# Optimization experiments

Hardware: AMD Instinct MI355X
Metric: run time of the kernel (lower is better)

## Reference

```python
import jax, jax.numpy as jnp
import numpy as np

B, E, F = 16384, 128, 6
ITEM_V, CATE_V, HIST = 91718, 11, 50
I_IDX, J_IDX = np.triu_indices(F, k=1)  # 15 field pairs, loop order (0,1),(0,2),...
EPS = 1e-5


def _xavier(key, shape):
    fan_in, fan_out = shape[0], shape[-1]
    std = (2.0 / (fan_in + fan_out)) ** 0.5
    return std * jax.random.normal(key, shape, dtype=jnp.float32)


def setup_inputs() -> dict:
    key = jax.random.key(0)
    ks = jax.random.split(key, 20)
    inp = {
        'item_id': jax.random.randint(ks[0], (B,), 0, ITEM_V),
        'item_emb_d128': jax.random.normal(ks[1], (B, 128), dtype=jnp.float32),
        'likes_level': jax.random.randint(ks[2], (B,), 0, CATE_V),
        'views_level': jax.random.randint(ks[3], (B,), 0, CATE_V),
        'item_seq': jax.random.randint(ks[4], (B, HIST), 0, ITEM_V),
        # learned parameters
        'item_emb': 0.05 * jax.random.normal(ks[5], (ITEM_V, E), dtype=jnp.float32),
        'cate_emb': 0.05 * jax.random.normal(ks[6], (CATE_V, E), dtype=jnp.float32),
        'mm_W': _xavier(ks[7], (128, E)), 'mm_b': jnp.zeros((E,), jnp.float32),
        'ln_g': jnp.ones((E,), jnp.float32), 'ln_b': jnp.zeros((E,), jnp.float32),
        'se_W1': _xavier(ks[8], (F, F // 2)), 'se_b1': jnp.zeros((F // 2,), jnp.float32),
        'se_W2': _xavier(ks[9], (F // 2, F)), 'se_b2': jnp.zeros((F,), jnp.float32),
        'bi_W': _xavier(ks[10], (E, E)),
        'mlp_W1': _xavier(ks[11], (21 * E, 512)), 'mlp_b1': jnp.zeros((512,), jnp.float32),
        'bn1_g': jnp.ones((512,), jnp.float32), 'bn1_b': jnp.zeros((512,), jnp.float32),
        'bn1_rm': jnp.zeros((512,), jnp.float32), 'bn1_rv': jnp.ones((512,), jnp.float32),
        'mlp_W2': _xavier(ks[12], (512, 256)), 'mlp_b2': jnp.zeros((256,), jnp.float32),
        'bn2_g': jnp.ones((256,), jnp.float32), 'bn2_b': jnp.zeros((256,), jnp.float32),
        'bn2_rm': jnp.zeros((256,), jnp.float32), 'bn2_rv': jnp.ones((256,), jnp.float32),
        'mlp_W3': _xavier(ks[13], (256, 1)), 'mlp_b3': jnp.zeros((1,), jnp.float32),
    }
    return inp


def _forward(item_id, item_emb_d128, likes_level, views_level, item_seq,
             item_emb, cate_emb, mm_W, mm_b, ln_g, ln_b,
             se_W1, se_b1, se_W2, se_b2, bi_W,
             mlp_W1, mlp_b1, bn1_g, bn1_b, bn1_rm, bn1_rv,
             mlp_W2, mlp_b2, bn2_g, bn2_b, bn2_rm, bn2_rv,
             mlp_W3, mlp_b3):
    b = item_id.shape[0]
    tab = item_emb.at[0].set(0.0)  # padding_idx=0
    like_feat = cate_emb[likes_level]
    view_feat = cate_emb[views_level]
    item_feat = tab[item_id]
    # mm_proj: Linear -> LayerNorm -> ReLU
    mm = item_emb_d128 @ mm_W + mm_b
    mu = mm.mean(-1, keepdims=True)
    var = jnp.var(mm, axis=-1, keepdims=True)
    mm = jax.nn.relu((mm - mu) / jnp.sqrt(var + EPS) * ln_g + ln_b)
    # masked mean pooling over history
    seq_emb = tab[item_seq]                               # (B, HIST, E)
    valid = (item_seq != 0).astype(seq_emb.dtype)
    seq_sum = (seq_emb * valid[..., None]).sum(1)
    cnt = jnp.clip(valid.sum(1, keepdims=True), 1.0)
    hist_feat = seq_sum / cnt
    user_feat = jnp.zeros((b, E), seq_emb.dtype)
    x = jnp.stack([user_feat, like_feat, view_feat, item_feat, mm, hist_feat], axis=1)  # (B,6,E)
    # SENet
    z = x.mean(-1)
    w = jax.nn.sigmoid(jax.nn.relu(z @ se_W1 + se_b1) @ se_W2 + se_b2)
    xs = x * w[:, :, None]
    # bilinear 'all'
    xw = jnp.einsum('bfe,ed->bfd', xs, bi_W)
    p = xs[:, I_IDX, :] * xw[:, J_IDX, :]                 # (B,15,E)
    c = jnp.concatenate([xs.reshape(b, -1), p.reshape(b, -1)], axis=1)  # (B, 2688)
    # MLP head (eval mode: BN uses running stats, dropout off)
    h = c @ mlp_W1 + mlp_b1
    h = jax.nn.relu((h - bn1_rm) / jnp.sqrt(bn1_rv + EPS) * bn1_g + bn1_b)
    h = h @ mlp_W2 + mlp_b2
    h = jax.nn.relu((h - bn2_rm) / jnp.sqrt(bn2_rv + EPS) * bn2_g + bn2_b)
    logits = h @ mlp_W3 + mlp_b3
    return jax.nn.sigmoid(logits)[:, 0]


def reference(item_id, item_emb_d128, likes_level, views_level, item_seq,
              item_emb, cate_emb, mm_W, mm_b, ln_g, ln_b,
              se_W1, se_b1, se_W2, se_b2, bi_W,
              mlp_W1, mlp_b1, bn1_g, bn1_b, bn1_rm, bn1_rv,
              mlp_W2, mlp_b2, bn2_g, bn2_b, bn2_rm, bn2_rv,
              mlp_W3, mlp_b3):
    return _forward(item_id, item_emb_d128, likes_level, views_level, item_seq,
                    item_emb, cate_emb, mm_W, mm_b, ln_g, ln_b,
                    se_W1, se_b1, se_W2, se_b2, bi_W,
                    mlp_W1, mlp_b1, bn1_g, bn1_b, bn1_rm, bn1_rv,
                    mlp_W2, mlp_b2, bn2_g, bn2_b, bn2_rm, bn2_rv,
                    mlp_W3, mlp_b3)
```

## Files before the change

### kernel.cpp

```cpp
#include <hip/hip_runtime.h>
#include <hip/hip_bf16.h>

typedef __hip_bfloat16 bfloat;
typedef __bf16 bf16x8 __attribute__((ext_vector_type(8)));
typedef float f32x4 __attribute__((ext_vector_type(4)));

#define B_SZ   16384
#define E_DIM  128
#define HIST_L 50


__device__ __constant__ int ISL[10] = {0,0,0,0,1,1,1,2,2,3};

__device__ __forceinline__ void gl_lds16(const void* g, void* l) {
    __builtin_amdgcn_global_load_lds(
        (const __attribute__((address_space(1))) unsigned int*)g,
        (__attribute__((address_space(3))) unsigned int*)l, 16, 0, 0);
}

template<int TB>
__global__ __launch_bounds__(256) void feat_kernel(
    const int* __restrict__ item_id,
    const int* __restrict__ likes, const int* __restrict__ views,
    const int* __restrict__ seq,
    const void* __restrict__ item_tab, const float* __restrict__ cate_emb,
    const float* __restrict__ mm,
    const float* __restrict__ ln_g, const float* __restrict__ ln_b,
    const float* __restrict__ se_W1, const float* __restrict__ se_b1,
    const float* __restrict__ se_W2, const float* __restrict__ se_b2,
    bfloat* __restrict__ xs)
{
    const int tid = threadIdx.x;
    const int r   = tid >> 7;
    const int e   = tid & 127;
    const int b   = blockIdx.x * 2 + r;
    const int w   = tid >> 6;

    __shared__ float redh[2][4][128];
    __shared__ int   seq_s[2][64];
    __shared__ float lnred[4], lnred2[4];
    __shared__ float zred[5][4];
    __shared__ float wsh[2][6];
    __shared__ int   cnt_s[2];

    if (e < 64) seq_s[r][e] = (e < HIST_L) ? seq[(size_t)b * HIST_L + e] : 0;
    __syncthreads();

    const int iid = item_id[b];
    const float like_v = cate_emb[likes[b] * 128 + e];
    const float view_v = cate_emb[views[b] * 128 + e];
    float item_v;
    if (TB) {
        const bfloat* tb = (const bfloat*)item_tab;
        item_v = __bfloat162float(tb[(size_t)iid * 128 + e]);
    } else {
        const float* tf = (const float*)item_tab;
        float raw = tf[(size_t)iid * 128 + e];
        item_v = iid ? raw : 0.f;
    }
    const float acc = mm[(size_t)b * 128 + e];

    const int q   = e >> 5;
    const int l32 = e & 31;
    float4 hs = make_float4(0.f, 0.f, 0.f, 0.f);
    if (TB) {
        const ushort* tb = (const ushort*)item_tab;
        #pragma unroll
        for (int g = 0; g < 13; ++g) {
            int s = seq_s[r][g * 4 + q];
            ushort4 v = *(const ushort4*)&tb[(size_t)s * 128 + l32 * 4];
            hs.x += __bfloat162float(__ushort_as_bfloat16(v.x));
            hs.y += __bfloat162float(__ushort_as_bfloat16(v.y));
            hs.z += __bfloat162float(__ushort_as_bfloat16(v.z));
            hs.w += __bfloat162float(__ushort_as_bfloat16(v.w));
        }
    } else {
        const float* tf = (const float*)item_tab;
        #pragma unroll
        for (int g = 0; g < 13; ++g) {
            int s = seq_s[r][g * 4 + q];
            const float4 v = *(const float4*)&tf[(size_t)s * 128 + l32 * 4];
            float m = (s != 0) ? 1.f : 0.f;
            hs.x = fmaf(v.x, m, hs.x);
            hs.y = fmaf(v.y, m, hs.y);
            hs.z = fmaf(v.z, m, hs.z);
            hs.w = fmaf(v.w, m, hs.w);
        }
    }

    {
        float v = acc;
        #pragma unroll
        for (int off = 32; off > 0; off >>= 1) v += __shfl_down(v, off, 64);
        if ((tid & 63) == 0) lnred[w] = v;
    }
    __syncthreads();
    const float mu = (lnred[2 * r] + lnred[2 * r + 1]) * (1.f / 128.f);
    const float d  = acc - mu;
    {
        float v = d * d;
        #pragma unroll
        for (int off = 32; off > 0; off >>= 1) v += __shfl_down(v, off, 64);
        if ((tid & 63) == 0) lnred2[w] = v;
    }
    redh[r][q][l32 * 4 + 0] = hs.x;
    redh[r][q][l32 * 4 + 1] = hs.y;
    redh[r][q][l32 * 4 + 2] = hs.z;
    redh[r][q][l32 * 4 + 3] = hs.w;
    if ((w & 1) == 0 && e < 64) {
        bool valid = (e < HIST_L) && (seq_s[r][e] != 0);
        unsigned long long m = __ballot(valid);
        if (e == 0) cnt_s[r] = (int)__popcll(m);
    }
    __syncthreads();
    const float var = (lnred2[2 * r] + lnred2[2 * r + 1]) * (1.f / 128.f);
    float xmm = d * rsqrtf(var + 1e-5f) * ln_g[e] + ln_b[e];
    xmm = fmaxf(xmm, 0.f);

    const int cnt = cnt_s[r] > 0 ? cnt_s[r] : 1;
    const float hist_v = (redh[r][0][e] + redh[r][1][e] +
                          redh[r][2][e] + redh[r][3][e]) / (float)cnt;

    {
        float s1 = like_v, s2 = view_v, s3 = item_v, s4 = xmm, s5 = hist_v;
        #pragma unroll
        for (int off = 32; off > 0; off >>= 1) {
            s1 += __shfl_down(s1, off, 64);
            s2 += __shfl_down(s2, off, 64);
            s3 += __shfl_down(s3, off, 64);
            s4 += __shfl_down(s4, off, 64);
            s5 += __shfl_down(s5, off, 64);
        }
        if ((tid & 63) == 0) {
            zred[0][w] = s1; zred[1][w] = s2; zred[2][w] = s3;
            zred[3][w] = s4; zred[4][w] = s5;
        }
    }
    __syncthreads();

    if (e == 0) {
        float z[6];
        z[0] = 0.f;
        #pragma unroll
        for (int f = 1; f < 6; ++f)
            z[f] = (zred[f - 1][2 * r] + zred[f - 1][2 * r + 1]) * (1.f / 128.f);
        float a[3];
        #pragma unroll
        for (int j = 0; j < 3; ++j) {
            float s = se_b1[j];
            #pragma unroll
            for (int f = 0; f < 6; ++f) s += z[f] * se_W1[f * 3 + j];
            a[j] = fmaxf(s, 0.f);
        }
        #pragma unroll
        for (int f = 0; f < 6; ++f) {
            float s = se_b2[f];
            #pragma unroll
            for (int j = 0; j < 3; ++j) s += a[j] * se_W2[j * 6 + f];
            wsh[r][f] = 1.f / (1.f + expf(-s));
        }
    }
    __syncthreads();

    bfloat* xrow = xs + (size_t)b * 640;
    xrow[0 * 128 + e] = __float2bfloat16(like_v * wsh[r][1]);
    xrow[1 * 128 + e] = __float2bfloat16(view_v * wsh[r][2]);
    xrow[2 * 128 + e] = __float2bfloat16(item_v * wsh[r][3]);
    xrow[3 * 128 + e] = __float2bfloat16(xmm    * wsh[r][4]);
    xrow[4 * 128 + e] = __float2bfloat16(hist_v * wsh[r][5]);
}

__global__ __launch_bounds__(256) void transpose_W1c(
    const float* __restrict__ W1, bfloat* __restrict__ W1t)
{
    __shared__ float t[64][65];
    const int tid = threadIdx.x;
    const int kk0 = blockIdx.x * 64, n0 = blockIdx.y * 64;
    const int j = tid & 63;
    #pragma unroll
    for (int p = 0; p < 16; ++p) {
        int i = (tid >> 6) + p * 4;
        int kk = kk0 + i;
        int orig = kk + (kk < 640 ? 128 : 768);
        t[i][j] = W1[(size_t)orig * 512 + n0 + j];
    }
    __syncthreads();
    #pragma unroll
    for (int p = 0; p < 16; ++p) {
        int i = (tid >> 6) + p * 4;
        W1t[(size_t)(n0 + i) * 1920 + kk0 + j] = __float2bfloat16(t[j][i]);
    }
}

__global__ __launch_bounds__(256) void prep_kernel(
    const float* __restrict__ W2, const float* __restrict__ bi_W,
    const float* __restrict__ mm_W,
    bfloat* __restrict__ W2t, bfloat* __restrict__ bWt,
    bfloat* __restrict__ mmWt,
    const float* __restrict__ lb1, const float* __restrict__ g1,
    const float* __restrict__ bb1, const float* __restrict__ rm1,
    const float* __restrict__ rv1,
    const float* __restrict__ lb2, const float* __restrict__ g2,
    const float* __restrict__ bb2, const float* __restrict__ rm2,
    const float* __restrict__ rv2,
    const float* __restrict__ mm_b,
    float* __restrict__ S1, float* __restrict__ T1,
    float* __restrict__ S2, float* __restrict__ T2,
    float* __restrict__ Tmm)
{
    int idx = blockIdx.x * 256 + threadIdx.x;
    if (idx < 131072) {
        int k = idx >> 8, n = idx & 255;
        W2t[(size_t)n * 512 + k] = __float2bfloat16(W2[idx]);
    } else if (idx < 147456) {
        int t = idx - 131072;
        int k = t >> 7, n = t & 127;
        bWt[n * 128 + k] = __float2bfloat16(bi_W[t]);
    } else if (idx < 163840) {
        int t = idx - 147456;
        int k = t >> 7, n = t & 127;
        mmWt[n * 128 + k] = __float2bfloat16(mm_W[t]);
    } else if (idx < 164352) {
        int j = idx - 163840;
        float s = g1[j] * rsqrtf(rv1[j] + 1e-5f);
        S1[j] = s;
        T1[j] = (lb1[j] - rm1[j]) * s + bb1[j];
    } else if (idx < 164608) {
        int j = idx - 164352;
        float s = g2[j] * rsqrtf(rv2[j] + 1e-5f);
        S2[j] = s;
        T2[j] = (lb2[j] - rm2[j]) * s + bb2[j];
    } else if (idx < 164736) {
        int j = idx - 164608;
        Tmm[j] = mm_b[j];
    }
}

__global__ __launch_bounds__(256) void cvt_emb(
    const float* __restrict__ in, bfloat* __restrict__ out, int n8)
{
    int idx = blockIdx.x * 256 + threadIdx.x;
    if (idx >= n8) return;
    if (idx < 16) {
        union { bf16x8 v; unsigned short s[8]; } z;
        #pragma unroll
        for (int i = 0; i < 8; ++i) z.s[i] = 0;
        ((bf16x8*)out)[idx] = z.v;
        return;
    }
    float4 f0 = ((const float4*)in)[idx * 2];
    float4 f1 = ((const float4*)in)[idx * 2 + 1];
    union { bf16x8 v; unsigned short s[8]; } u;
    u.s[0] = __bfloat16_as_ushort(__float2bfloat16(f0.x));
    u.s[1] = __bfloat16_as_ushort(__float2bfloat16(f0.y));
    u.s[2] = __bfloat16_as_ushort(__float2bfloat16(f0.z));
    u.s[3] = __bfloat16_as_ushort(__float2bfloat16(f0.w));
    u.s[4] = __bfloat16_as_ushort(__float2bfloat16(f1.x));
    u.s[5] = __bfloat16_as_ushort(__float2bfloat16(f1.y));
    u.s[6] = __bfloat16_as_ushort(__float2bfloat16(f1.z));
    u.s[7] = __bfloat16_as_ushort(__float2bfloat16(f1.w));
    ((bf16x8*)out)[idx] = u.v;
}

__global__ __launch_bounds__(256, 1) void gemm_mlp1(
    const bfloat* __restrict__ Axs, const bfloat* __restrict__ Ap,
    const bfloat* __restrict__ Bt, bfloat* __restrict__ C,
    int M, int N, int K,
    const float* __restrict__ S, const float* __restrict__ T)
{
    extern __shared__ __align__(16) short smem[];

    const int tid  = threadIdx.x;
    const int bm   = blockIdx.x * 256;
    const int bn   = blockIdx.y * 128;
    const int wave = tid >> 6;
    const int lane = tid & 63;
    const int wm   = (wave >> 1) * 128;
    const int wn   = (wave & 1) * 64;

    const short* Ag  = (const short*)Axs;
    const short* A2g = (const short*)Ap;
    const short* Bg  = (const short*)Bt;

    f32x4 acc[8][4];
    #pragma unroll
    for (int i = 0; i < 8; ++i)
        #pragma unroll
        for (int j = 0; j < 4; ++j)
            acc[i][j] = (f32x4){0.f, 0.f, 0.f, 0.f};

    const int l8  = lane >> 3;
    const int gch = (lane & 7) ^ l8;

    auto stage = [&](int buf, int kt) {
        short* Ab = smem + buf * 24576;
        short* Bb = Ab + 16384;
        #pragma unroll
        for (int d = 0; d < 4; ++d) {
            int seg = wave * 4 + d;
            int row = seg * 8 + l8;
            gl_lds16(&Bg[(long)(bn + row) * K + kt + gch * 8],
                     &Bb[seg * 512 + lane * 8]);
        }
        #pragma unroll
        for (int d = 0; d < 8; ++d) {
            int seg = wave * 8 + d;
            int row = seg * 8 + l8;
            long rb = (long)(bm + row);
            const short* src = (kt < 640)
                ? &Ag [rb * 640  + kt + gch * 8]
                : &A2g[rb * 1280 + (kt - 640) + gch * 8];
            gl_lds16(src, &Ab[seg * 512 + lane * 8]);
        }
    };

    const int rbase = lane & 15;
    const int rsw   = rbase & 7;

    const int nk = K >> 6;
    stage(0, 0);
    stage(1, 64);

    for (int i = 0; i < nk; ++i) {
        if (i + 1 < nk) asm volatile("s_waitcnt vmcnt(12)" ::: "memory");
        else            asm volatile("s_waitcnt vmcnt(0)" ::: "memory");
        __builtin_amdgcn_s_barrier();
        __builtin_amdgcn_sched_barrier(0);

        if (i + 2 < nk) stage((i + 2) % 3, (i + 2) << 6);

        const short* Ab = smem + (i % 3) * 24576;
        const short* Bb = Ab + 16384;
        #pragma unroll
        for (int h = 0; h < 2; ++h) {
            const int cg = h * 4 + (lane >> 4);
            const int ca = (cg ^ rsw) << 3;
            bf16x8 af[8], bfr[4];
            #pragma unroll
            for (int mt = 0; mt < 8; ++mt)
                af[mt] = *(const bf16x8*)
                    &Ab[(wm + mt * 16 + rbase) * 64 + ca];
            #pragma unroll
            for (int nt = 0; nt < 4; ++nt)
                bfr[nt] = *(const bf16x8*)
                    &Bb[(wn + nt * 16 + rbase) * 64 + ca];
            #pragma unroll
            for (int mt = 0; mt < 8; ++mt)
                #pragma unroll
                for (int nt = 0; nt < 4; ++nt)
                    acc[mt][nt] = __builtin_amdgcn_mfma_f32_16x16x32_bf16(
                        af[mt], bfr[nt], acc[mt][nt], 0, 0, 0);
        }
    }

    const int col0 = lane & 15;
    const int row0 = (lane >> 4) * 4;
    #pragma unroll
    for (int nt = 0; nt < 4; ++nt) {
        int col = bn + wn + nt * 16 + col0;
        float s = S[col], t = T[col];
        #pragma unroll
        for (int mt = 0; mt < 8; ++mt) {
            #pragma unroll
            for (int i = 0; i < 4; ++i) {
                int row = bm + wm + mt * 16 + row0 + i;
                float v = fmaxf(acc[mt][nt][i] * s + t, 0.f);
                C[(size_t)row * N + col] = __float2bfloat16(v);
            }
        }
    }
}

template<int MODE, int EPI, int F32OUT>
__global__ __launch_bounds__(256, 2) void gemm_bt(
    const void* __restrict__ A, const bfloat* __restrict__ A2,
    const bfloat* __restrict__ Bt, void* __restrict__ C,
    int M, int N, int K,
    const float* __restrict__ S, const float* __restrict__ T)
{
    __shared__ __align__(16) short As[4][128 * 32];
    __shared__ __align__(16) short Bs[4][128 * 32];

    const int tid  = threadIdx.x;
    const int bm   = blockIdx.x * 128;
    const int bn   = blockIdx.y * 128;
    const int wave = tid >> 6;
    const int lane = tid & 63;
    const int wm   = (wave >> 1) * 64;
    const int wn   = (wave & 1) * 64;

    const short* Ag  = (const short*)A;
    const short* A2g = (const short*)A2;
    const short* Bg  = (const short*)Bt;

    f32x4 acc[4][4];
    #pragma unroll
    for (int i = 0; i < 4; ++i)
        #pragma unroll
        for (int j = 0; j < 4; ++j)
            acc[i][j] = (f32x4){0.f, 0.f, 0.f, 0.f};

    const int srow = tid >> 2;
    const int sck  = tid & 3;

    auto stage = [&](int buf, int kt) {
        #pragma unroll
        for (int rr = 0; rr < 2; ++rr) {
            int row = srow + rr * 64;
            int g   = sck ^ ((row >> 1) & 3);
            gl_lds16(&Bg[(long)(bn + row) * K + kt + g * 8],
                     &Bs[buf][row * 32 + sck * 8]);
        }
        if (MODE == 3) {
            const float* Af = (const float*)A;
            #pragma unroll
            for (int rr = 0; rr < 2; ++rr) {
                int row = srow + rr * 64;
                int g   = sck ^ ((row >> 1) & 3);
                long aoff = (long)(bm + row) * K + kt + g * 8;
                float4 f0 = *(const float4*)&Af[aoff];
                float4 f1 = *(const float4*)&Af[aoff + 4];
                union { bf16x8 v; unsigned short s[8]; } u;
                u.s[0] = __bfloat16_as_ushort(__float2bfloat16(f0.x));
                u.s[1] = __bfloat16_as_ushort(__float2bfloat16(f0.y));
                u.s[2] = __bfloat16_as_ushort(__float2bfloat16(f0.z));
                u.s[3] = __bfloat16_as_ushort(__float2bfloat16(f0.w));
                u.s[4] = __bfloat16_as_ushort(__float2bfloat16(f1.x));
                u.s[5] = __bfloat16_as_ushort(__float2bfloat16(f1.y));
                u.s[6] = __bfloat16_as_ushort(__float2bfloat16(f1.z));
                u.s[7] = __bfloat16_as_ushort(__float2bfloat16(f1.w));
                *(bf16x8*)&As[buf][row * 32 + sck * 8] = u.v;
            }
        } else {
            #pragma unroll
            for (int rr = 0; rr < 2; ++rr) {
                int row = srow + rr * 64;
                int g   = sck ^ ((row >> 1) & 3);
                const short* src;
                if (MODE == 2) {
                    int gr = bm + row;
                    src = &Ag[((long)(gr >> 2)) * 640 +
                              ((gr & 3) + 1) * 128 + kt + g * 8];
                } else {
                    src = &Ag[(long)(bm + row) * K + kt + g * 8];
                }
                gl_lds16(src, &As[buf][row * 32 + sck * 8]);
            }
        }
    };

    const int rbase = lane & 15;
    const int cg    = lane >> 4;
    const int ca    = (cg ^ ((rbase >> 1) & 3)) << 3;

    const int nk = K >> 5;
    stage(0, 0);
    stage(1, 32);
    if (nk > 2) stage(2, 64);

    for (int i = 0; i < nk; ++i) {
        if (MODE == 3)
            asm volatile("s_waitcnt vmcnt(0) lgkmcnt(0)" ::: "memory");
        else if (i + 2 < nk)
            asm volatile("s_waitcnt vmcnt(8)" ::: "memory");
        else if (i + 1 < nk)
            asm volatile("s_waitcnt vmcnt(4)" ::: "memory");
        else
            asm volatile("s_waitcnt vmcnt(0)" ::: "memory");
        __builtin_amdgcn_s_barrier();
        __builtin_amdgcn_sched_barrier(0);

        const int cur = i & 3;
        bf16x8 af[4], bfr[4];
        #pragma unroll
        for (int mt = 0; mt < 4; ++mt)
            af[mt] = *(const bf16x8*)
                &As[cur][(wm + mt * 16 + rbase) * 32 + ca];
        #pragma unroll
        for (int nt = 0; nt < 4; ++nt)
            bfr[nt] = *(const bf16x8*)
                &Bs[cur][(wn + nt * 16 + rbase) * 32 + ca];
        #pragma unroll
        for (int mt = 0; mt < 4; ++mt)
            #pragma unroll
            for (int nt = 0; nt < 4; ++nt)
                acc[mt][nt] = __builtin_amdgcn_mfma_f32_16x16x32_bf16(
                    af[mt], bfr[nt], acc[mt][nt], 0, 0, 0);

        if (i + 3 < nk) stage((i + 3) & 3, (i + 3) << 5);
    }

    const int col0 = lane & 15;
    const int row0 = (lane >> 4) * 4;
    #pragma unroll
    for (int nt = 0; nt < 4; ++nt) {
        int col = bn + wn + nt * 16 + col0;
        float s = 1.f, t = 0.f;
        if (EPI == 1 || EPI == 2) { s = (EPI == 1) ? S[col] : 1.f; t = T[col]; }
        #pragma unroll
        for (int mt = 0; mt < 4; ++mt) {
            #pragma unroll
            for (int i = 0; i < 4; ++i) {
                int row = bm + wm + mt * 16 + row0 + i;
                float v = acc[mt][nt][i];
                if (EPI == 3) {
                    const bfloat* xsp = (const bfloat*)A;
                    bfloat* Pp = (bfloat*)C;
                    long b = row >> 2;
                    int pplist[4];
                    int npp;
                    if (i == 0)      { npp = 1; pplist[0] = 0; }
                    else if (i == 1) { npp = 2; pplist[0] = 1; pplist[1] = 4; }
                    else if (i == 2) { npp = 3; pplist[0] = 2; pplist[1] = 5; pplist[2] = 7; }
                    else             { npp = 4; pplist[0] = 3; pplist[1] = 6; pplist[2] = 8; pplist[3] = 9; }
                    #pragma unroll
                    for (int t2 = 0; t2 < npp; ++t2) {
                        int pp  = pplist[t2];
                        int isl = ISL[pp];
                        float xv = __bfloat162float(
                            xsp[b * 640 + isl * 128 + col]);
                        Pp[b * 1280 + pp * 128 + col] =
                            __float2bfloat16(xv * v);
                    }
                } else {
                    if (EPI == 1) v = fmaxf(v * s + t, 0.f);
                    if (EPI == 2) v = v + t;
                    if (F32OUT) ((float*)C)[(size_t)row * N + col] = v;
                    else ((bfloat*)C)[(size_t)row * N + col] = __float2bfloat16(v);
                }
            }
        }
    }
}

__global__ __launch_bounds__(256) void head_kernel(
    const bfloat* __restrict__ h2, const float* __restrict__ W3,
    const float* __restrict__ b3, float* __restrict__ out)
{
    int lane = threadIdx.x & 63;
    int row  = blockIdx.x * 4 + (threadIdx.x >> 6);
    float acc = 0.f;
    #pragma unroll
    for (int i = 0; i < 4; ++i)
        acc += __bfloat162float(h2[(size_t)row * 256 + i * 64 + lane]) *
               W3[i * 64 + lane];
    #pragma unroll
    for (int off = 32; off > 0; off >>= 1) acc += __shfl_down(acc, off, 64);
    if (lane == 0) {
        float l = acc + b3[0];
        out[row] = 1.f / (1.f + expf(-l));
    }
}

extern "C" void kernel_launch(void* const* d_in, const int* in_sizes, int n_in,
                              void* d_out, int out_size, void* d_ws, size_t ws_size,
                              hipStream_t stream) {
    const int*   item_id = (const int*)  d_in[0];
    const float* d128    = (const float*)d_in[1];
    const int*   likes   = (const int*)  d_in[2];
    const int*   views   = (const int*)  d_in[3];
    const int*   seq     = (const int*)  d_in[4];
    const float* item_emb= (const float*)d_in[5];
    const float* cate_emb= (const float*)d_in[6];
    const float* mm_W    = (const float*)d_in[7];
    const float* mm_b    = (const float*)d_in[8];
    const float* ln_g    = (const float*)d_in[9];
    const float* ln_b    = (const float*)d_in[10];
    const float* se_W1   = (const float*)d_in[11];
    const float* se_b1   = (const float*)d_in[12];
    const float* se_W2   = (const float*)d_in[13];
    const float* se_b2   = (const float*)d_in[14];
    const float* bi_W    = (const float*)d_in[15];
    const float* W1      = (const float*)d_in[16];
    const float* b1      = (const float*)d_in[17];
    const float* bn1_g   = (const float*)d_in[18];
    const float* bn1_b   = (const float*)d_in[19];
    const float* bn1_rm  = (const float*)d_in[20];
    const float* bn1_rv  = (const float*)d_in[21];
    const float* W2      = (const float*)d_in[22];
    const float* b2      = (const float*)d_in[23];
    const float* bn2_g   = (const float*)d_in[24];
    const float* bn2_b   = (const float*)d_in[25];
    const float* bn2_rm  = (const float*)d_in[26];
    const float* bn2_rv  = (const float*)d_in[27];
    const float* W3      = (const float*)d_in[28];
    const float* b3      = (const float*)d_in[29];

    const size_t fixed = 2300416;
    const size_t ITB   = 23479808;
    int CH; bool use_tb;
    if      (fixed + ITB + (size_t)16384 * 4864 <= ws_size) { CH = 16384; use_tb = true;  }
    else if (fixed + (size_t)16384 * 4864 <= ws_size)       { CH = 16384; use_tb = false; }
    else if (fixed + ITB + (size_t)8192 * 4864 <= ws_size)  { CH = 8192;  use_tb = true;  }
    else if (fixed + (size_t)8192 * 4864 <= ws_size)        { CH = 8192;  use_tb = false; }
    else if (fixed + ITB + (size_t)4096 * 4864 <= ws_size)  { CH = 4096;  use_tb = true;  }
    else if (fixed + (size_t)4096 * 4864 <= ws_size)        { CH = 4096;  use_tb = false; }
    else if (fixed + (size_t)2048 * 4864 <= ws_size)        { CH = 2048;  use_tb = false; }
    else                                                    { CH = 1024;  use_tb = false; }

    char* ws = (char*)d_ws;
    bfloat* W1t = (bfloat*)(ws);
    bfloat* W2t = (bfloat*)(ws + 1966080);
    bfloat* bWt = (bfloat*)(ws + 2228224);
    bfloat* mmWt= (bfloat*)(ws + 2260992);
    float*  S1  = (float*) (ws + 2293760);
    float*  T1  = (float*) (ws + 2295808);
    float*  S2  = (float*) (ws + 2297856);
    float*  T2  = (float*) (ws + 2298880);
    float*  Tmm = (float*) (ws + 2299904);
    bfloat* itemb = (bfloat*)(ws + fixed);
    char*   cb  = ws + fixed + (use_tb ? ITB : 0);
    bfloat* xs  = (bfloat*)(cb);
    bfloat* h1  = (bfloat*)(cb + (size_t)CH * 1280);
    bfloat* P   = (bfloat*)(cb + (size_t)CH * 2304);
    float*  mm  = (float*)P;
    bfloat* h2  = (bfloat*)P;

    transpose_W1c<<<dim3(30, 8), 256, 0, stream>>>(W1, W1t);
    prep_kernel<<<(164736 + 255) / 256, 256, 0, stream>>>(
        W2, bi_W, mm_W, W2t, bWt, mmWt,
        b1, bn1_g, bn1_b, bn1_rm, bn1_rv,
        b2, bn2_g, bn2_b, bn2_rm, bn2_rv,
        mm_b, S1, T1, S2, T2, Tmm);
    if (use_tb) {
        const int n8 = 91718 * 128 / 8;
        cvt_emb<<<(n8 + 255) / 256, 256, 0, stream>>>(item_emb, itemb, n8);
    }

    for (int off = 0; off < B_SZ; off += CH) {
        dim3 gmm(CH / 128, 1);
        gemm_bt<3, 2, 1><<<gmm, 256, 0, stream>>>(
            d128 + (size_t)off * 128, nullptr, mmWt, mm,
            CH, 128, 128, nullptr, Tmm);

        if (use_tb)
            feat_kernel<1><<<CH / 2, 256, 0, stream>>>(
                item_id + off, likes + off, views + off,
                seq + (size_t)off * HIST_L, itemb, cate_emb, mm,
                ln_g, ln_b, se_W1, se_b1, se_W2, se_b2, xs);
        else
            feat_kernel<0><<<CH / 2, 256, 0, stream>>>(
                item_id + off, likes + off, views + off,
                seq + (size_t)off * HIST_L, item_emb, cate_emb, mm,
                ln_g, ln_b, se_W1, se_b1, se_W2, se_b2, xs);

        dim3 gxw(CH * 4 / 128, 1);
        gemm_bt<2, 3, 0><<<gxw, 256, 0, stream>>>(
            xs, nullptr, bWt, P, CH * 4, 128, 128, nullptr, nullptr);

        dim3 g1(CH / 256, 4);
        gemm_mlp1<<<g1, 256, 147456, stream>>>(
            xs, P, W1t, h1, CH, 512, 1920, S1, T1);

        dim3 g2(CH / 128, 2);
        gemm_bt<0, 1, 0><<<g2, 256, 0, stream>>>(
            h1, nullptr, W2t, h2, CH, 256, 512, S2, T2);

        head_kernel<<<CH / 4, 256, 0, stream>>>(h2, W3, b3, (float*)d_out + off);
    }
}
```

Baseline: 278.1 us.

## Fuse mm projection into feat kernel and merge prep kernels into one launch

The separate MFMA GEMM that projects item_emb_d128 through mm_W is removed. Each feat_kernel thread now computes its output element as a scalar 128-long dot product against a bf16 transposed weight row, reading the input row from LDS. This drops a launch and the fp32 mm intermediate round-trip through memory. The three setup kernels (W1 transpose, weight/BN prep, embedding conversion) are merged into one launch to cut launch overhead. The cost is that the projection now runs on scalar FMA instead of matrix cores, with each thread reading a 256-byte weight row.

```diff
diff --git a/kernel.cpp b/kernel.cpp
--- a/kernel.cpp
+++ b/kernel.cpp
@@ -24,7 +24,8 @@
     const int* __restrict__ likes, const int* __restrict__ views,
     const int* __restrict__ seq,
     const void* __restrict__ item_tab, const float* __restrict__ cate_emb,
-    const float* __restrict__ mm,
+    const float* __restrict__ d128, const bfloat* __restrict__ mmWt,
+    const float* __restrict__ mm_b,
     const float* __restrict__ ln_g, const float* __restrict__ ln_b,
     const float* __restrict__ se_W1, const float* __restrict__ se_b1,
     const float* __restrict__ se_W2, const float* __restrict__ se_b2,
@@ -37,6 +38,7 @@
     const int w   = tid >> 6;
 
     __shared__ float redh[2][4][128];
+    __shared__ float d128s[2][128];
     __shared__ int   seq_s[2][64];
     __shared__ float lnred[4], lnred2[4];
     __shared__ float zred[5][4];
@@ -44,6 +46,7 @@
     __shared__ int   cnt_s[2];
 
     if (e < 64) seq_s[r][e] = (e < HIST_L) ? seq[(size_t)b * HIST_L + e] : 0;
+    d128s[r][e] = d128[(size_t)b * 128 + e];
     __syncthreads();
 
     const int iid = item_id[b];
@@ -58,7 +61,6 @@
         float raw = tf[(size_t)iid * 128 + e];
         item_v = iid ? raw : 0.f;
     }
-    const float acc = mm[(size_t)b * 128 + e];
 
     const int q   = e >> 5;
     const int l32 = e & 31;
@@ -88,6 +90,22 @@
         }
     }
 
+    float acc = mm_b[e];
+    {
+        const ushort* wrow = (const ushort*)(mmWt + (size_t)e * 128);
+        #pragma unroll
+        for (int k8 = 0; k8 < 16; ++k8) {
+            union { bf16x8 v; ushort s[8]; } u;
+            u.v = *(const bf16x8*)&wrow[k8 * 8];
+            const float* dp = &d128s[r][k8 * 8];
+            #pragma unroll
+            for (int j = 0; j < 8; ++j)
+                acc = fmaf(dp[j],
+                           __bfloat162float(__ushort_as_bfloat16(u.s[j])),
+                           acc);
+        }
+    }
+
     {
         float v = acc;
         #pragma unroll
@@ -170,29 +188,8 @@
     xrow[4 * 128 + e] = __float2bfloat16(hist_v * wsh[r][5]);
 }
 
-__global__ __launch_bounds__(256) void transpose_W1c(
-    const float* __restrict__ W1, bfloat* __restrict__ W1t)
-{
-    __shared__ float t[64][65];
-    const int tid = threadIdx.x;
-    const int kk0 = blockIdx.x * 64, n0 = blockIdx.y * 64;
-    const int j = tid & 63;
-    #pragma unroll
-    for (int p = 0; p < 16; ++p) {
-        int i = (tid >> 6) + p * 4;
-        int kk = kk0 + i;
-        int orig = kk + (kk < 640 ? 128 : 768);
-        t[i][j] = W1[(size_t)orig * 512 + n0 + j];
-    }
-    __syncthreads();
-    #pragma unroll
-    for (int p = 0; p < 16; ++p) {
-        int i = (tid >> 6) + p * 4;
-        W1t[(size_t)(n0 + i) * 1920 + kk0 + j] = __float2bfloat16(t[j][i]);
-    }
-}
-
-__global__ __launch_bounds__(256) void prep_kernel(
+__global__ __launch_bounds__(256) void mega_prep(
+    const float* __restrict__ W1, bfloat* __restrict__ W1t,
     const float* __restrict__ W2, const float* __restrict__ bi_W,
     const float* __restrict__ mm_W,
     bfloat* __restrict__ W2t, bfloat* __restrict__ bWt,
@@ -203,63 +200,78 @@
     const float* __restrict__ lb2, const float* __restrict__ g2,
     const float* __restrict__ bb2, const float* __restrict__ rm2,
     const float* __restrict__ rv2,
-    const float* __restrict__ mm_b,
     float* __restrict__ S1, float* __restrict__ T1,
     float* __restrict__ S2, float* __restrict__ T2,
-    float* __restrict__ Tmm)
+    const float* __restrict__ item_emb, bfloat* __restrict__ itemb)
 {
-    int idx = blockIdx.x * 256 + threadIdx.x;
-    if (idx < 131072) {
-        int k = idx >> 8, n = idx & 255;
-        W2t[(size_t)n * 512 + k] = __float2bfloat16(W2[idx]);
-    } else if (idx < 147456) {
-        int t = idx - 131072;
-        int k = t >> 7, n = t & 127;
-        bWt[n * 128 + k] = __float2bfloat16(bi_W[t]);
-    } else if (idx < 163840) {
-        int t = idx - 147456;
-        int k = t >> 7, n = t & 127;
-        mmWt[n * 128 + k] = __float2bfloat16(mm_W[t]);
-    } else if (idx < 164352) {
-        int j = idx - 163840;
-        float s = g1[j] * rsqrtf(rv1[j] + 1e-5f);
-        S1[j] = s;
-        T1[j] = (lb1[j] - rm1[j]) * s + bb1[j];
-    } else if (idx < 164608) {
-        int j = idx - 164352;
-        float s = g2[j] * rsqrtf(rv2[j] + 1e-5f);
-        S2[j] = s;
-        T2[j] = (lb2[j] - rm2[j]) * s + bb2[j];
-    } else if (idx < 164736) {
-        int j = idx - 164608;
-        Tmm[j] = mm_b[j];
-    }
-}
-
-__global__ __launch_bounds__(256) void cvt_emb(
-    const float* __restrict__ in, bfloat* __restrict__ out, int n8)
-{
-    int idx = blockIdx.x * 256 + threadIdx.x;
-    if (idx >= n8) return;
-    if (idx < 16) {
-        union { bf16x8 v; unsigned short s[8]; } z;
-        #pragma unroll
-        for (int i = 0; i < 8; ++i) z.s[i] = 0;
-        ((bf16x8*)out)[idx] = z.v;
-        return;
-    }
-    float4 f0 = ((const float4*)in)[idx * 2];
-    float4 f1 = ((const float4*)in)[idx * 2 + 1];
-    union { bf16x8 v; unsigned short s[8]; } u;
-    u.s[0] = __bfloat16_as_ushort(__float2bfloat16(f0.x));
-    u.s[1] = __bfloat16_as_ushort(__float2bfloat16(f0.y));
-    u.s[2] = __bfloat16_as_ushort(__float2bfloat16(f0.z));
-    u.s[3] = __bfloat16_as_ushort(__float2bfloat16(f0.w));
-    u.s[4] = __bfloat16_as_ushort(__float2bfloat16(f1.x));
-    u.s[5] = __bfloat16_as_ushort(__float2bfloat16(f1.y));
-    u.s[6] = __bfloat16_as_ushort(__float2bfloat16(f1.z));
-    u.s[7] = __bfloat16_as_ushort(__float2bfloat16(f1.w));
-    ((bf16x8*)out)[idx] = u.v;
+    const int blk = blockIdx.x;
+    const int tid = threadIdx.x;
+    if (blk < 240) {
+        __shared__ float t[64][65];
+        const int kk0 = (blk % 30) * 64, n0 = (blk / 30) * 64;
+        const int j = tid & 63;
+        #pragma unroll
+        for (int p = 0; p < 16; ++p) {
+            int i = (tid >> 6) + p * 4;
+            int kk = kk0 + i;
+            int orig = kk + (kk < 640 ? 128 : 768);
+            t[i][j] = W1[(size_t)orig * 512 + n0 + j];
+        }
+        __syncthreads();
+        #pragma unroll
+        for (int p = 0; p < 16; ++p) {
+            int i = (tid >> 6) + p * 4;
+            W1t[(size_t)(n0 + i) * 1920 + kk0 + j] = __float2bfloat16(t[j][i]);
+        }
+    } else if (blk < 884) {
+        int idx = (blk - 240) * 256 + tid;
+        if (idx < 131072) {
+            int k = idx >> 8, n = idx & 255;
+            W2t[(size_t)n * 512 + k] = __float2bfloat16(W2[idx]);
+        } else if (idx < 147456) {
+            int t2 = idx - 131072;
+            int k = t2 >> 7, n = t2 & 127;
+            bWt[n * 128 + k] = __float2bfloat16(bi_W[t2]);
+        } else if (idx < 163840) {
+            int t2 = idx - 147456;
+            int k = t2 >> 7, n = t2 & 127;
+            mmWt[n * 128 + k] = __float2bfloat16(mm_W[t2]);
+        } else if (idx < 164352) {
+            int j = idx - 163840;
+            float s = g1[j] * rsqrtf(rv1[j] + 1e-5f);
+            S1[j] = s;
+            T1[j] = (lb1[j] - rm1[j]) * s + bb1[j];
+        } else if (idx < 164608) {
+            int j = idx - 164352;
+            float s = g2[j] * rsqrtf(rv2[j] + 1e-5f);
+            S2[j] = s;
+            T2[j] = (lb2[j] - rm2[j]) * s + bb2[j];
+        }
+    } else {
+        if (itemb == nullptr) return;
+        const int n8 = 91718 * 128 / 8;
+        int idx = (blk - 884) * 256 + tid;
+        if (idx >= n8) return;
+        if (idx < 16) {
+            union { bf16x8 v; unsigned short s[8]; } z;
+            #pragma unroll
+            for (int i = 0; i < 8; ++i) z.s[i] = 0;
+            ((bf16x8*)itemb)[idx] = z.v;
+            return;
+        }
+        float4 f0 = ((const float4*)item_emb)[idx * 2];
+        float4 f1 = ((const float4*)item_emb)[idx * 2 + 1];
+        union { bf16x8 v; unsigned short s[8]; } u;
+        u.s[0] = __bfloat16_as_ushort(__float2bfloat16(f0.x));
+        u.s[1] = __bfloat16_as_ushort(__float2bfloat16(f0.y));
+        u.s[2] = __bfloat16_as_ushort(__float2bfloat16(f0.z));
+        u.s[3] = __bfloat16_as_ushort(__float2bfloat16(f0.w));
+        u.s[4] = __bfloat16_as_ushort(__float2bfloat16(f1.x));
+        u.s[5] = __bfloat16_as_ushort(__float2bfloat16(f1.y));
+        u.s[6] = __bfloat16_as_ushort(__float2bfloat16(f1.z));
+        u.s[7] = __bfloat16_as_ushort(__float2bfloat16(f1.w));
+        ((bf16x8*)itemb)[idx] = u.v;
+    }
 }
 
 __global__ __launch_bounds__(256, 1) void gemm_mlp1(
@@ -390,7 +402,6 @@
     const int wn   = (wave & 1) * 64;
 
     const short* Ag  = (const short*)A;
-    const short* A2g = (const short*)A2;
     const short* Bg  = (const short*)Bt;
 
     f32x4 acc[4][4];
@@ -411,41 +422,19 @@
             gl_lds16(&Bg[(long)(bn + row) * K + kt + g * 8],
                      &Bs[buf][row * 32 + sck * 8]);
         }
-        if (MODE == 3) {
-            const float* Af = (const float*)A;
-            #pragma unroll
-            for (int rr = 0; rr < 2; ++rr) {
-                int row = srow + rr * 64;
-                int g   = sck ^ ((row >> 1) & 3);
-                long aoff = (long)(bm + row) * K + kt + g * 8;
-                float4 f0 = *(const float4*)&Af[aoff];
-                float4 f1 = *(const float4*)&Af[aoff + 4];
-                union { bf16x8 v; unsigned short s[8]; } u;
-                u.s[0] = __bfloat16_as_ushort(__float2bfloat16(f0.x));
-                u.s[1] = __bfloat16_as_ushort(__float2bfloat16(f0.y));
-                u.s[2] = __bfloat16_as_ushort(__float2bfloat16(f0.z));
-                u.s[3] = __bfloat16_as_ushort(__float2bfloat16(f0.w));
-                u.s[4] = __bfloat16_as_ushort(__float2bfloat16(f1.x));
-                u.s[5] = __bfloat16_as_ushort(__float2bfloat16(f1.y));
-                u.s[6] = __bfloat16_as_ushort(__float2bfloat16(f1.z));
-                u.s[7] = __bfloat16_as_ushort(__float2bfloat16(f1.w));
-                *(bf16x8*)&As[buf][row * 32 + sck * 8] = u.v;
+        #pragma unroll
+        for (int rr = 0; rr < 2; ++rr) {
+            int row = srow + rr * 64;
+            int g   = sck ^ ((row >> 1) & 3);
+            const short* src;
+            if (MODE == 2) {
+                int gr = bm + row;
+                src = &Ag[((long)(gr >> 2)) * 640 +
+                          ((gr & 3) + 1) * 128 + kt + g * 8];
+            } else {
+                src = &Ag[(long)(bm + row) * K + kt + g * 8];
             }
-        } else {
-            #pragma unroll
-            for (int rr = 0; rr < 2; ++rr) {
-                int row = srow + rr * 64;
-                int g   = sck ^ ((row >> 1) & 3);
-                const short* src;
-                if (MODE == 2) {
-                    int gr = bm + row;
-                    src = &Ag[((long)(gr >> 2)) * 640 +
-                              ((gr & 3) + 1) * 128 + kt + g * 8];
-                } else {
-                    src = &Ag[(long)(bm + row) * K + kt + g * 8];
-                }
-                gl_lds16(src, &As[buf][row * 32 + sck * 8]);
-            }
+            gl_lds16(src, &As[buf][row * 32 + sck * 8]);
         }
     };
 
@@ -459,9 +448,7 @@
     if (nk > 2) stage(2, 64);
 
     for (int i = 0; i < nk; ++i) {
-        if (MODE == 3)
-            asm volatile("s_waitcnt vmcnt(0) lgkmcnt(0)" ::: "memory");
-        else if (i + 2 < nk)
+        if (i + 2 < nk)
             asm volatile("s_waitcnt vmcnt(8)" ::: "memory");
         else if (i + 1 < nk)
             asm volatile("s_waitcnt vmcnt(4)" ::: "memory");
@@ -607,41 +594,35 @@
     float*  T1  = (float*) (ws + 2295808);
     float*  S2  = (float*) (ws + 2297856);
     float*  T2  = (float*) (ws + 2298880);
-    float*  Tmm = (float*) (ws + 2299904);
     bfloat* itemb = (bfloat*)(ws + fixed);
     char*   cb  = ws + fixed + (use_tb ? ITB : 0);
     bfloat* xs  = (bfloat*)(cb);
     bfloat* h1  = (bfloat*)(cb + (size_t)CH * 1280);
     bfloat* P   = (bfloat*)(cb + (size_t)CH * 2304);
-    float*  mm  = (float*)P;
     bfloat* h2  = (bfloat*)P;
 
-    transpose_W1c<<<dim3(30, 8), 256, 0, stream>>>(W1, W1t);
-    prep_kernel<<<(164736 + 255) / 256, 256, 0, stream>>>(
-        W2, bi_W, mm_W, W2t, bWt, mmWt,
-        b1, bn1_g, bn1_b, bn1_rm, bn1_rv,
-        b2, bn2_g, bn2_b, bn2_rm, bn2_rv,
-        mm_b, S1, T1, S2, T2, Tmm);
-    if (use_tb) {
-        const int n8 = 91718 * 128 / 8;
-        cvt_emb<<<(n8 + 255) / 256, 256, 0, stream>>>(item_emb, itemb, n8);
+    {
+        int nblk = 884 + (use_tb ? (91718 * 128 / 8 + 255) / 256 : 0);
+        mega_prep<<<nblk, 256, 0, stream>>>(
+            W1, W1t, W2, bi_W, mm_W, W2t, bWt, mmWt,
+            b1, bn1_g, bn1_b, bn1_rm, bn1_rv,
+            b2, bn2_g, bn2_b, bn2_rm, bn2_rv,
+            S1, T1, S2, T2,
+            item_emb, use_tb ? itemb : nullptr);
     }
 
     for (int off = 0; off < B_SZ; off += CH) {
-        dim3 gmm(CH / 128, 1);
-        gemm_bt<3, 2, 1><<<gmm, 256, 0, stream>>>(
-            d128 + (size_t)off * 128, nullptr, mmWt, mm,
-            CH, 128, 128, nullptr, Tmm);
-
         if (use_tb)
             feat_kernel<1><<<CH / 2, 256, 0, stream>>>(
                 item_id + off, likes + off, views + off,
-                seq + (size_t)off * HIST_L, itemb, cate_emb, mm,
+                seq + (size_t)off * HIST_L, itemb, cate_emb,
+                d128 + (size_t)off * 128, mmWt, mm_b,
                 ln_g, ln_b, se_W1, se_b1, se_W2, se_b2, xs);
         else
             feat_kernel<0><<<CH / 2, 256, 0, stream>>>(
                 item_id + off, likes + off, views + off,
-                seq + (size_t)off * HIST_L, item_emb, cate_emb, mm,
+                seq + (size_t)off * HIST_L, item_emb, cate_emb,
+                d128 + (size_t)off * 128, mmWt, mm_b,
                 ln_g, ln_b, se_W1, se_b1, se_W2, se_b2, xs);
 
         dim3 gxw(CH * 4 / 128, 1);
```

Result: slower. 315.8 us (+13.5%).
